# Kernel tuning notes

Hardware: AMD Instinct MI355X
Metric: run time of the kernel (lower is better)

The kernel has to match this reference:

```python
import jax, jax.numpy as jnp
import numpy as np

V_THRESH = 0.3

@jax.custom_vjp
def spike(x):
    return (x > 0).astype(x.dtype)

def _spike_fwd(x):
    return spike(x), x

def _spike_bwd(x, g):
    # rectangular straight-through surrogate gradient (pass grad where |x| < 0.5)
    return (g * (jnp.abs(x) < 0.5).astype(g.dtype),)

spike.defvjp(_spike_fwd, _spike_bwd)


def setup_inputs() -> dict:
    key = jax.random.key(0)
    B, T, H = 128, 2048, 128
    k1, = jax.random.split(key, 1)
    x_seq = jax.random.normal(k1, (B, T, H), dtype=jnp.float32)
    v0 = jnp.zeros((B, H), dtype=jnp.float32)
    z0 = jnp.zeros((B, H), dtype=jnp.float32)
    decay_raw = jnp.zeros((H,), dtype=jnp.float32)  # nn.initializers.constant(0.0)
    return {"x_seq": x_seq, "v0": v0, "z0": z0, "decay_raw": decay_raw}


def reference(x_seq, v0, z0, decay_raw):
    # LIF recurrence: v_t = v_{t-1} * decay * (1 - z_{t-1}) + x_t ; z_t = spike(v_t - v_thresh)
    decay = jax.nn.sigmoid(decay_raw)  # (H,)

    def step(carry, x_t):
        v, z = carry
        v = v * decay * (1.0 - z) + x_t
        z_out = spike(v - V_THRESH)
        return (v, z_out), z_out

    x_tb = jnp.swapaxes(x_seq, 0, 1)  # [T, B, H] for lax.scan over time
    (_, _), spk_tb = jax.lax.scan(step, (v0, z0), x_tb)
    return jnp.swapaxes(spk_tb, 0, 1)  # [B, T, H]
```

## Files before the change

### kernel.cpp

```cpp
#include <hip/hip_runtime.h>
#include <math.h>


constexpr int Bdim = 128;
constexpr int Tdim = 2048;
constexpr int Hdim = 128;
constexpr int HW   = 64;
constexpr int Ut   = 64;
constexpr int NT   = Tdim / Ut;
constexpr int NX   = 8;
constexpr int NLOAD = 7;
constexpr float VTH = 0.3f;

__device__ __forceinline__ void lgkm_fence() {
    asm volatile("s_waitcnt lgkmcnt(0)" ::: "memory");
}

__global__ __launch_bounds__(512) void lif_kernel(
    const float* __restrict__ x,
    const float* __restrict__ v0,
    const float* __restrict__ z0,
    const float* __restrict__ decay_raw,
    float* __restrict__ out)
{
    __shared__ float    xbuf[NX][Ut][HW];
    __shared__ unsigned zbits[Tdim / 32][HW];
    __shared__ int      flags[NT + 4];

    volatile int* vf = (volatile int*)flags;

    const int tid  = threadIdx.x;
    const int wave = tid >> 6;
    const int lane = tid & 63;
    const int blk  = blockIdx.x;
    const int b    = blk >> 1;
    const int h0   = (blk & 1) * HW;

    for (int i = tid; i < NT + 4; i += 512) flags[i] = 0;
    __syncthreads();

    for (int i = 0; i < (blk & 3); ++i) __builtin_amdgcn_s_sleep(16);

    const float* xbase = x   + (size_t)b * Tdim * Hdim + h0;
    float*       obase = out + (size_t)b * Tdim * Hdim + h0;
    const int r_sub = lane >> 4;
    const int c_sub = (lane & 15) * 4;
    const int sub   = r_sub * Hdim + c_sub;

    if (wave >= 1) {
        for (int k = wave - 1; k < NT; k += NLOAD) {
            while (vf[NT] < k - (NX - 1)) __builtin_amdgcn_s_sleep(2);
            const float* g = xbase + (size_t)k * Ut * Hdim + sub;
            float4 tmp[16];
            #pragma unroll
            for (int j = 0; j < 16; ++j)
                tmp[j] = *(const float4*)(g + (size_t)(4 * j) * Hdim);
            const int xb = k % NX;
            #pragma unroll
            for (int j = 0; j < 16; ++j)
                *(float4*)&xbuf[xb][4 * j + r_sub][c_sub] = tmp[j];
            lgkm_fence();
            if (lane == 0) vf[k] = 1;
        }
    } else {
        const float decay = 1.0f / (1.0f + expf(-decay_raw[h0 + lane]));
        float v = v0[b * Hdim + h0 + lane];
        float z = z0[b * Hdim + h0 + lane];

        for (int k = 0; k < NT; ++k) {
            while (vf[k] == 0) __builtin_amdgcn_s_sleep(1);
            const int xb = k % NX;
            #pragma unroll
            for (int w32 = 0; w32 < Ut / 32; ++w32) {
                unsigned mask = 0u;
                #pragma unroll
                for (int tb = 0; tb < 32; ++tb) {
                    const int t = w32 * 32 + tb;
                    const float xv = xbuf[xb][t][lane];
                    const float s  = v * decay + xv;
                    v = (z > 0.5f) ? xv : s;
                    const bool sp = (v > VTH);
                    z = sp ? 1.0f : 0.0f;
                    mask |= (sp ? 1u : 0u) << tb;
                }
                zbits[k * (Ut / 32) + w32][lane] = mask;
            }
            lgkm_fence();
            if (lane == 0) vf[NT] = k + 1;
        }
    }

    __syncthreads();

    {
        const int t0 = wave * (Tdim / 8);
        #pragma unroll 8
        for (int t = t0; t < t0 + Tdim / 8; ++t) {
            const unsigned word = zbits[t >> 5][lane];
            const float f = ((word >> (t & 31)) & 1u) ? 1.0f : 0.0f;
            obase[(size_t)t * Hdim + lane] = f;
        }
    }
}

extern "C" void kernel_launch(void* const* d_in, const int* in_sizes, int n_in,
                              void* d_out, int out_size, void* d_ws, size_t ws_size,
                              hipStream_t stream) {
    const float* x         = (const float*)d_in[0];
    const float* v0        = (const float*)d_in[1];
    const float* z0        = (const float*)d_in[2];
    const float* decay_raw = (const float*)d_in[3];
    float* out = (float*)d_out;

    lif_kernel<<<Bdim * Hdim / HW, 512, 0, stream>>>(x, v0, z0, decay_raw, out);
}
```

Before: 246.5 us.

## Replace flag-based producer/consumer waves with single-wave register double-buffered pipeline

Blocks shrink from 8 waves to a single wave. Instead of 7 loader waves filling an 8-slot LDS ring and signalling the compute wave through flags, the one wave prefetches upcoming tiles into registers, stages them into a 2-slot LDS buffer, and runs the recurrence in between. This removes flag polling, sleep loops and the heavy LDS footprint, but it cuts per-block memory parallelism and moves the whole output write onto one wave. Prefetch depth drops to about two tiles, and with only 256 single-wave blocks latency hiding may suffer.

```diff
diff --git a/kernel.cpp b/kernel.cpp
--- a/kernel.cpp
+++ b/kernel.cpp
@@ -8,38 +8,22 @@
 constexpr int HW   = 64;
 constexpr int Ut   = 64;
 constexpr int NT   = Tdim / Ut;
-constexpr int NX   = 8;
-constexpr int NLOAD = 7;
 constexpr float VTH = 0.3f;
 
-__device__ __forceinline__ void lgkm_fence() {
-    asm volatile("s_waitcnt lgkmcnt(0)" ::: "memory");
-}
-
-__global__ __launch_bounds__(512) void lif_kernel(
+__global__ __launch_bounds__(64, 1) void lif_kernel(
     const float* __restrict__ x,
     const float* __restrict__ v0,
     const float* __restrict__ z0,
     const float* __restrict__ decay_raw,
     float* __restrict__ out)
 {
-    __shared__ float    xbuf[NX][Ut][HW];
+    __shared__ float    xslot[2][Ut][HW];
     __shared__ unsigned zbits[Tdim / 32][HW];
-    __shared__ int      flags[NT + 4];
 
-    volatile int* vf = (volatile int*)flags;
-
-    const int tid  = threadIdx.x;
-    const int wave = tid >> 6;
-    const int lane = tid & 63;
+    const int lane = threadIdx.x;
     const int blk  = blockIdx.x;
     const int b    = blk >> 1;
     const int h0   = (blk & 1) * HW;
-
-    for (int i = tid; i < NT + 4; i += 512) flags[i] = 0;
-    __syncthreads();
-
-    for (int i = 0; i < (blk & 3); ++i) __builtin_amdgcn_s_sleep(16);
 
     const float* xbase = x   + (size_t)b * Tdim * Hdim + h0;
     float*       obase = out + (size_t)b * Tdim * Hdim + h0;
@@ -47,59 +31,61 @@
     const int c_sub = (lane & 15) * 4;
     const int sub   = r_sub * Hdim + c_sub;
 
-    if (wave >= 1) {
-        for (int k = wave - 1; k < NT; k += NLOAD) {
-            while (vf[NT] < k - (NX - 1)) __builtin_amdgcn_s_sleep(2);
-            const float* g = xbase + (size_t)k * Ut * Hdim + sub;
-            float4 tmp[16];
+    const float decay = 1.0f / (1.0f + expf(-decay_raw[h0 + lane]));
+    float v = v0[b * Hdim + h0 + lane];
+    float z = z0[b * Hdim + h0 + lane];
+
+    float4 A[16], B[16];
+
+    auto loadT = [&](int tile, float4 (&buf)[16]) {
+        const float* g = xbase + (size_t)tile * Ut * Hdim + sub;
+        #pragma unroll
+        for (int j = 0; j < 16; ++j)
+            buf[j] = *(const float4*)(g + (size_t)(4 * j) * Hdim);
+    };
+    auto stageT = [&](int slot, float4 (&buf)[16]) {
+        #pragma unroll
+        for (int j = 0; j < 16; ++j)
+            *(float4*)&xslot[slot][4 * j + r_sub][c_sub] = buf[j];
+    };
+    auto compT = [&](int k, int slot) {
+        #pragma unroll
+        for (int w = 0; w < 2; ++w) {
+            unsigned mask = 0u;
             #pragma unroll
-            for (int j = 0; j < 16; ++j)
-                tmp[j] = *(const float4*)(g + (size_t)(4 * j) * Hdim);
-            const int xb = k % NX;
-            #pragma unroll
-            for (int j = 0; j < 16; ++j)
-                *(float4*)&xbuf[xb][4 * j + r_sub][c_sub] = tmp[j];
-            lgkm_fence();
-            if (lane == 0) vf[k] = 1;
+            for (int tb = 0; tb < 32; ++tb) {
+                const float xv = xslot[slot][w * 32 + tb][lane];
+                const float s  = v * decay + xv;
+                v = (z > 0.5f) ? xv : s;
+                const bool sp = (v > VTH);
+                z = sp ? 1.0f : 0.0f;
+                mask |= (sp ? 1u : 0u) << tb;
+            }
+            zbits[k * 2 + w][lane] = mask;
         }
-    } else {
-        const float decay = 1.0f / (1.0f + expf(-decay_raw[h0 + lane]));
-        float v = v0[b * Hdim + h0 + lane];
-        float z = z0[b * Hdim + h0 + lane];
+    };
 
-        for (int k = 0; k < NT; ++k) {
-            while (vf[k] == 0) __builtin_amdgcn_s_sleep(1);
-            const int xb = k % NX;
-            #pragma unroll
-            for (int w32 = 0; w32 < Ut / 32; ++w32) {
-                unsigned mask = 0u;
-                #pragma unroll
-                for (int tb = 0; tb < 32; ++tb) {
-                    const int t = w32 * 32 + tb;
-                    const float xv = xbuf[xb][t][lane];
-                    const float s  = v * decay + xv;
-                    v = (z > 0.5f) ? xv : s;
-                    const bool sp = (v > VTH);
-                    z = sp ? 1.0f : 0.0f;
-                    mask |= (sp ? 1u : 0u) << tb;
-                }
-                zbits[k * (Ut / 32) + w32][lane] = mask;
-            }
-            lgkm_fence();
-            if (lane == 0) vf[NT] = k + 1;
-        }
+    loadT(0, A);
+    loadT(1, B);
+    stageT(0, A);
+
+    #pragma unroll 1
+    for (int k = 0; k < NT; k += 2) {
+        if (k + 2 < NT) loadT(k + 2, A);
+        stageT(1, B);
+        compT(k, 0);
+        if (k + 3 < NT) loadT(k + 3, B);
+        if (k + 2 < NT) stageT(0, A);
+        compT(k + 1, 1);
     }
 
-    __syncthreads();
-
-    {
-        const int t0 = wave * (Tdim / 8);
-        #pragma unroll 8
-        for (int t = t0; t < t0 + Tdim / 8; ++t) {
-            const unsigned word = zbits[t >> 5][lane];
-            const float f = ((word >> (t & 31)) & 1u) ? 1.0f : 0.0f;
-            obase[(size_t)t * Hdim + lane] = f;
-        }
+    #pragma unroll 2
+    for (int tw = 0; tw < Tdim / 32; ++tw) {
+        const unsigned word = zbits[tw][lane];
+        float* op = obase + (size_t)tw * 32 * Hdim + lane;
+        #pragma unroll
+        for (int tb = 0; tb < 32; ++tb)
+            op[(size_t)tb * Hdim] = ((word >> tb) & 1u) ? 1.0f : 0.0f;
     }
 }
 
@@ -112,5 +98,5 @@
     const float* decay_raw = (const float*)d_in[3];
     float* out = (float*)d_out;
 
-    lif_kernel<<<Bdim * Hdim / HW, 512, 0, stream>>>(x, v0, z0, decay_raw, out);
+    lif_kernel<<<Bdim * Hdim / HW, 64, 0, stream>>>(x, v0, z0, decay_raw, out);
 }
```

Result: slower. 285.4 us (+15.8%).
